# Optimization experiments

Hardware: AMD Instinct MI355X
Metric: run time of the kernel (lower is better)

The kernel has to match this reference:

```python
import jax, jax.numpy as jnp
import numpy as np

# ----- static configuration (from init_kwargs) -----
M = 129                      # NpointsMesh (odd)
XLIMS = (0.0, 2.0 * np.pi)
L = abs(XLIMS[1] - XLIMS[0])
TAU = 12.0 * (L / (2.0 * np.pi * M)) ** 2
MU0 = 1.0
MU1 = 1.0
PI = np.pi

_kGrid = (2.0 * np.pi / L) * np.linspace(-(M // 2), M // 2, M).astype(np.float32)
_KY, _KX = np.meshgrid(_kGrid, _kGrid)            # tf.meshgrid 'xy': ky[i,j]=k[j], kx[i,j]=k[i]
KX = jnp.asarray(_KX, jnp.float32)
KY = jnp.asarray(_KY, jnp.float32)
_xGrid = np.linspace(XLIMS[0], XLIMS[1], M + 1)[:-1].astype(np.float32)
_YG, _XG = np.meshgrid(_xGrid, _xGrid)
XG = jnp.asarray(_XG, jnp.float32)
YG = jnp.asarray(_YG, jnp.float32)


def gaussian_per(x, tau=TAU, Lp=L):
    # periodic Gaussian: main image + two periodic images
    inv = 1.0 / (4.0 * tau)
    return (jnp.exp(-jnp.square(x) * inv)
            + jnp.exp(-jnp.square(x - Lp) * inv)
            + jnp.exp(-jnp.square(x + Lp) * inv))


def setup_inputs() -> dict:
    key = jax.random.key(0)
    kx, = jax.random.split(key, 1)
    B, NP = 4, 512
    x = jax.random.uniform(kx, (B, NP, 2), dtype=jnp.float32) * L  # points in [0, 2pi)
    ones = jnp.ones((1,), jnp.float32)
    return {"x": x, "shift0": ones, "shift1": ones, "amp0": ones, "amp1": ones}


def reference(x, shift0, shift1, amp0, amp1):
    # Gaussian spreading onto the mesh: [B, Np, M, M]
    diffx = x[:, :, 0][..., None, None] - XG
    diffy = x[:, :, 1][..., None, None] - YG
    g = gaussian_per(diffx) * gaussian_per(diffy)

    # NUFFT: FFT of spread Gaussians, centered spectrum
    G = jnp.fft.fftshift(jnp.fft.fft2(g.astype(jnp.complex64)), axes=(-2, -1))
    # deconvolution of the Gaussian window
    deconv = (PI / TAU) * jnp.exp((jnp.square(KX) + jnp.square(KY)) * TAU)  # [M,M] real
    rfft = G * deconv

    k2 = jnp.square(KX) + jnp.square(KY)
    scale = 1.0 / ((2.0 * PI * M / L) ** 2) / ((2.0 * PI) ** 2) / 2.0

    def channel_energy(amp, shift, mu):
        mult = amp * 4.0 * PI / (k2 + jnp.square(mu * shift))   # [M,M] real (broadcast of [1])
        mfft = rfft * mult * deconv                              # second deconvolution
        irfft = jnp.real(jnp.fft.ifft2(jnp.fft.ifftshift(mfft, axes=(-2, -1)))) * scale
        diag = jnp.sum(irfft * g, axis=(-2, -1))                             # [B, Np]
        total = jnp.sum(jnp.sum(irfft, axis=1, keepdims=True) * g, axis=(-2, -1))
        return total - diag

    e1 = channel_energy(amp0, shift0, MU0)
    e2 = channel_energy(amp1, shift1, MU1)
    return jnp.stack([e1, e2], axis=-1)   # [B, Np, 2]
```

## Files before the change

### kernel.cpp

```cpp
#include <hip/hip_runtime.h>
#include <math.h>

#define MM 129
#define KP 132
#define NP 512
#define NB 4
#define NPC 16
#define PCHUNK (NP / NPC)

static constexpr double D_PI  = 3.14159265358979323846;
static constexpr double D_L   = 2.0 * D_PI;
static constexpr double D_TAU = 12.0 / ((double)MM * (double)MM);
static constexpr double D_INV4TAU = 1.0 / (4.0 * D_TAU);
static constexpr double D_F = 1.0 / (8.0 * D_PI * D_PI * (double)MM * (double)MM * (double)MM * (double)MM);

__device__ __forceinline__ void cmac(float2& acc, float2 a, float2 b) {
    acc.x = fmaf(a.x, b.x, fmaf(-a.y, b.y, acc.x));
    acc.y = fmaf(a.x, b.y, fmaf( a.y, b.x, acc.y));
}

#define PPB 2
__global__ __launch_bounds__(128) void k_dft(const float* __restrict__ x,
                                             float2* __restrict__ A,
                                             float2* __restrict__ B) {
    const int p0  = blockIdx.x * PPB;
    const int tid = threadIdx.x;

    __shared__ float4 sG[MM];
    __shared__ float red[2][8];

    const float inv4tau = (float)D_INV4TAU;
    const float Lf      = (float)D_L;
    for (int idx = tid; idx < MM * PPB; idx += 128) {
        int pt = idx & 1, a = idx >> 1;
        float x0 = x[(p0 + pt) * 2 + 0];
        float x1 = x[(p0 + pt) * 2 + 1];
        float u  = (float)a * (float)(D_L / MM);
        float d0 = x0 - u, d1 = x1 - u;
        float ga = __expf(-d0 * d0 * inv4tau)
                 + __expf(-(d0 - Lf) * (d0 - Lf) * inv4tau)
                 + __expf(-(d0 + Lf) * (d0 + Lf) * inv4tau);
        float gb = __expf(-d1 * d1 * inv4tau)
                 + __expf(-(d1 - Lf) * (d1 - Lf) * inv4tau)
                 + __expf(-(d1 + Lf) * (d1 + Lf) * inv4tau);
        ((float2*)&sG[a])[pt] = make_float2(ga, gb);
    }
    __syncthreads();

    const int pt = tid & 1;
    const int j  = tid >> 1;
    const int kk = 64 + j;
    const float nf = (float)(-2.0 * D_PI / MM);

    float sw, cw;
    __sincosf(nf * (float)j, &sw, &cw);
    const int step16 = (j * 16) % MM;
    int idx = 0;

    float Ar = 0.f, Ai = 0.f, Br = 0.f, Bi = 0.f;
    for (int c = 0; c < 128; c += 16) {
        float st, ct;
        __sincosf(nf * (float)idx, &st, &ct);
        float tx = ct, ty = st;
        #pragma unroll
        for (int q = 0; q < 16; ++q) {
            float2 g = ((const float2*)&sG[c + q])[pt];
            Ar = fmaf(g.x, tx, Ar); Ai = fmaf(g.x, ty, Ai);
            Br = fmaf(g.y, tx, Br); Bi = fmaf(g.y, ty, Bi);
            float nx = fmaf(tx, cw, -(ty * sw));
            float ny = fmaf(tx, sw,   ty * cw);
            tx = nx; ty = ny;
        }
        idx += step16; if (idx >= MM) idx -= MM;
    }
    {
        float st, ct;
        __sincosf(nf * (float)idx, &st, &ct);
        float2 g = ((const float2*)&sG[128])[pt];
        Ar = fmaf(g.x, ct, Ar); Ai = fmaf(g.x, st, Ai);
        Br = fmaf(g.y, ct, Br); Bi = fmaf(g.y, st, Bi);
    }

    {
        const size_t base = (size_t)(p0 + pt) * KP;
        A[base + kk] = make_float2(Ar, Ai);
        B[base + kk] = make_float2(Br, Bi);
        if (j > 0) {
            A[base + 64 - j] = make_float2(Ar, -Ai);
            B[base + 64 - j] = make_float2(Br, -Bi);
        }
    }

    const int lane = tid & 63, wv = tid >> 6;
    float2 t1, t128;
    {
        int ph = (64 * tid) % MM;
        __sincosf(nf * (float)ph, &t1.y, &t1.x);
        __sincosf(nf * 65.f, &t128.y, &t128.x);
    }
    float4 gt   = sG[tid];
    float4 g128 = sG[128];
    #pragma unroll
    for (int p = 0; p < PPB; ++p) {
        float ga = p ? gt.z : gt.x;
        float gb = p ? gt.w : gt.y;
        float ar = ga * t1.x, ai = ga * t1.y;
        float br = gb * t1.x, bi = gb * t1.y;
        if (tid == 0) {
            float ga8 = p ? g128.z : g128.x;
            float gb8 = p ? g128.w : g128.y;
            ar = fmaf(ga8, t128.x, ar); ai = fmaf(ga8, t128.y, ai);
            br = fmaf(gb8, t128.x, br); bi = fmaf(gb8, t128.y, bi);
        }
        #pragma unroll
        for (int o = 32; o > 0; o >>= 1) {
            ar += __shfl_down(ar, o, 64); ai += __shfl_down(ai, o, 64);
            br += __shfl_down(br, o, 64); bi += __shfl_down(bi, o, 64);
        }
        if (lane == 0) {
            red[wv][p * 4 + 0] = ar; red[wv][p * 4 + 1] = ai;
            red[wv][p * 4 + 2] = br; red[wv][p * 4 + 3] = bi;
        }
    }
    __syncthreads();
    if (tid < 4) {
        int p = tid >> 1, isB = tid & 1;
        float re = red[0][p * 4 + isB * 2 + 0] + red[1][p * 4 + isB * 2 + 0];
        float im = red[0][p * 4 + isB * 2 + 1] + red[1][p * 4 + isB * 2 + 1];
        float2* dst = isB ? B : A;
        const size_t base = (size_t)(p0 + p) * KP;
        dst[base + 128] = make_float2(re, im);
        dst[base + 0]   = make_float2(re, -im);
    }
}

__global__ __launch_bounds__(128) void k_s1(const float2* __restrict__ A,
                                            const float2* __restrict__ B,
                                            float2* __restrict__ P) {
    const int b   = blockIdx.z;
    const int pc  = blockIdx.y;
    const int p0  = pc * PCHUNK;
    const int m0  = blockIdx.x * 4;
    const int tid = threadIdx.x;

    const float2* __restrict__ Ab = A + (size_t)b * NP * KP;
    const float2* __restrict__ Bb = B + (size_t)b * NP * KP;

    float2 acc[4];
    #pragma unroll
    for (int i = 0; i < 4; ++i) acc[i] = make_float2(0.f, 0.f);
    float2 acc2 = make_float2(0.f, 0.f);

    float2 v[4], am[4][4], as[4], bu[4];
    #pragma unroll
    for (int i = 0; i < 4; ++i) {
        const size_t r = (size_t)(p0 + i) * KP;
        v[i]  = Bb[r + tid];
        bu[i] = Bb[r + 128];
        as[i] = Ab[r + m0 + (tid & 3)];
        #pragma unroll
        for (int j = 0; j < 4; ++j) am[i][j] = Ab[r + m0 + j];
    }

    for (int pg = 0; pg < PCHUNK; pg += 4) {
        float2 nv[4], nam[4][4], nas[4], nbu[4];
        const bool more = (pg + 4 < PCHUNK);
        if (more) {
            #pragma unroll
            for (int i = 0; i < 4; ++i) {
                const size_t r = (size_t)(p0 + pg + 4 + i) * KP;
                nv[i]  = Bb[r + tid];
                nbu[i] = Bb[r + 128];
                nas[i] = Ab[r + m0 + (tid & 3)];
                #pragma unroll
                for (int j = 0; j < 4; ++j) nam[i][j] = Ab[r + m0 + j];
            }
        }
        #pragma unroll
        for (int i = 0; i < 4; ++i) {
            cmac(acc[0], am[i][0], v[i]);
            cmac(acc[1], am[i][1], v[i]);
            cmac(acc[2], am[i][2], v[i]);
            cmac(acc[3], am[i][3], v[i]);
        }
        if (tid < 4) {
            #pragma unroll
            for (int i = 0; i < 4; ++i) cmac(acc2, as[i], bu[i]);
        }
        if (more) {
            #pragma unroll
            for (int i = 0; i < 4; ++i) {
                v[i] = nv[i]; bu[i] = nbu[i]; as[i] = nas[i];
                #pragma unroll
                for (int j = 0; j < 4; ++j) am[i][j] = nam[i][j];
            }
        }
    }

    float2* Pb = P + ((size_t)(b * NPC + pc) * 68) * KP;
    #pragma unroll
    for (int i = 0; i < 4; ++i)
        Pb[(size_t)(m0 + i) * KP + tid] = acc[i];
    if (tid < 4)
        Pb[(size_t)(m0 + tid) * KP + 128] = acc2;
}

#define OUT_FLOATS (NB * NP * 2)
__global__ __launch_bounds__(256) void k_s2(const float2* __restrict__ P,
                                            float2* __restrict__ S,
                                            const float* __restrict__ s0p,
                                            const float* __restrict__ s1p,
                                            const float* __restrict__ a0p,
                                            const float* __restrict__ a1p,
                                            float2* __restrict__ Wp,
                                            float* __restrict__ out) {
    const int idx = blockIdx.x * 256 + threadIdx.x;

    if (idx < OUT_FLOATS) out[idx] = 0.f;

    if (idx < 65 * KP) {
        int m = idx / KP, n = idx - (idx / KP) * KP;
        float w0 = 0.f, w1 = 0.f;
        if (n < MM) {
            float kx = (float)(m - 64), ky = (float)(n - 64);
            float k2   = kx * kx + ky * ky;
            float dec  = (float)(D_PI / D_TAU) * expf(k2 * (float)D_TAU);
            float base = dec * dec * (float)(4.0 * D_PI * D_F);
            float s0 = s0p[0], s1 = s1p[0];
            w0 = a0p[0] * base / (k2 + s0 * s0);
            w1 = a1p[0] * base / (k2 + s1 * s1);
        }
        Wp[idx] = make_float2(w0, w1);
    }

    if (idx < NB * 68 * KP) {
        const int b   = idx / (68 * KP);
        const int rem = idx - b * (68 * KP);
        const int m   = rem / KP;
        const int n   = rem - m * KP;
        if (n <= 128) {
            const float2* __restrict__ Pb =
                P + ((size_t)b * NPC * 68) * KP + (size_t)m * KP + n;
            float re = 0.f, im = 0.f;
            #pragma unroll
            for (int pc = 0; pc < NPC; ++pc) {
                float2 vv = Pb[(size_t)pc * 68 * KP];
                re += vv.x; im += vv.y;
            }
            S[(size_t)b * KP * KP + (size_t)m * KP + n] = make_float2(re, im);
        }
    }
}

__global__ __launch_bounds__(128) void k_final(const float2* __restrict__ A,
                                               const float2* __restrict__ B,
                                               const float2* __restrict__ S,
                                               const float2* __restrict__ Wp,
                                               float* __restrict__ out) {
    const int b      = blockIdx.z;
    const int mc     = blockIdx.y;
    const int mstart = mc * 8;
    const int p0     = blockIdx.x * 8;
    const int tid    = threadIdx.x;

    __shared__ float2 sA[8][65];
    __shared__ float2 sB[8][KP];
    for (int idx = tid; idx < 8 * 65; idx += 128) {
        int pi = idx / 65, k = idx - pi * 65;
        sA[pi][k] = A[(size_t)(b * NP + p0 + pi) * KP + k];
    }
    for (int idx = tid; idx < 8 * 129; idx += 128) {
        int pi = idx / 129, k = idx - pi * 129;
        sB[pi][k] = B[(size_t)(b * NP + p0 + pi) * KP + k];
    }
    __syncthreads();

    float2 bb[8];
    #pragma unroll
    for (int pi = 0; pi < 8; ++pi) bb[pi] = sB[pi][tid];

    float e0[8], e1[8];
    #pragma unroll
    for (int i = 0; i < 8; ++i) { e0[i] = 0.f; e1[i] = 0.f; }

    const float2* __restrict__ Sb = S + (size_t)b * KP * KP;
    float2 s = Sb[(size_t)mstart * KP + tid];
    float2 w = Wp[(size_t)mstart * KP + tid];
    #pragma unroll
    for (int mi = 0; mi < 8; ++mi) {
        const int m = mstart + mi;
        float2 sn = s, wn = w;
        if (mi < 7) {
            sn = Sb[(size_t)(m + 1) * KP + tid];
            wn = Wp[(size_t)(m + 1) * KP + tid];
        }
        #pragma unroll
        for (int pi = 0; pi < 8; ++pi) {
            float2 a  = sA[pi][m];
            float2 bv = bb[pi];
            float abr = a.x * bv.x - a.y * bv.y;
            float abi = a.x * bv.y + a.y * bv.x;
            float d   = fmaf(s.x, abr, s.y * abi) - fmaf(abr, abr, abi * abi);
            e0[pi] = fmaf(w.x, d, e0[pi]);
            e1[pi] = fmaf(w.y, d, e1[pi]);
        }
        s = sn; w = wn;
    }
    if (tid < 8) {
        const int m = mstart + tid;
        float2 s8 = Sb[(size_t)m * KP + 128];
        float2 w8 = Wp[(size_t)m * KP + 128];
        #pragma unroll
        for (int pi = 0; pi < 8; ++pi) {
            float2 a  = sA[pi][m];
            float2 bv = sB[pi][128];
            float abr = a.x * bv.x - a.y * bv.y;
            float abi = a.x * bv.y + a.y * bv.x;
            float d   = fmaf(s8.x, abr, s8.y * abi) - fmaf(abr, abr, abi * abi);
            e0[pi] = fmaf(w8.x, d, e0[pi]);
            e1[pi] = fmaf(w8.y, d, e1[pi]);
        }
    }
    #pragma unroll
    for (int i = 0; i < 8; ++i) { e0[i] *= 2.f; e1[i] *= 2.f; }

    if (mc == 7) {
        float wt = (tid < 64) ? 2.f : ((tid == 64) ? 1.f : 0.f);
        float2 s64 = Sb[(size_t)64 * KP + tid];
        float2 w64 = Wp[(size_t)64 * KP + tid];
        w64.x *= wt; w64.y *= wt;
        #pragma unroll
        for (int pi = 0; pi < 8; ++pi) {
            float2 a  = sA[pi][64];
            float2 bv = bb[pi];
            float abr = a.x * bv.x - a.y * bv.y;
            float abi = a.x * bv.y + a.y * bv.x;
            float d   = fmaf(s64.x, abr, s64.y * abi) - fmaf(abr, abr, abi * abi);
            e0[pi] = fmaf(w64.x, d, e0[pi]);
            e1[pi] = fmaf(w64.y, d, e1[pi]);
        }
    }

    const int lane = tid & 63, wv = tid >> 6;
    __shared__ float part[2][16];
    #pragma unroll
    for (int pi = 0; pi < 8; ++pi) {
        float r0 = e0[pi], r1 = e1[pi];
        #pragma unroll
        for (int o = 32; o > 0; o >>= 1) {
            r0 += __shfl_down(r0, o, 64);
            r1 += __shfl_down(r1, o, 64);
        }
        if (lane == 0) { part[wv][pi * 2 + 0] = r0; part[wv][pi * 2 + 1] = r1; }
    }
    __syncthreads();
    if (tid < 16) {
        float r = part[0][tid] + part[1][tid];
        int pi = tid >> 1, c = tid & 1;
        atomicAdd(&out[((size_t)(b * NP + p0 + pi)) * 2 + c], r);
    }
}

extern "C" void kernel_launch(void* const* d_in, const int* in_sizes, int n_in,
                              void* d_out, int out_size, void* d_ws, size_t ws_size,
                              hipStream_t stream) {
    const float* x      = (const float*)d_in[0];
    const float* shift0 = (const float*)d_in[1];
    const float* shift1 = (const float*)d_in[2];
    const float* amp0   = (const float*)d_in[3];
    const float* amp1   = (const float*)d_in[4];
    float* out = (float*)d_out;

    float2* A  = (float2*)d_ws;
    float2* Bv = A + (size_t)NB * NP * KP;
    float2* S  = Bv + (size_t)NB * NP * KP;
    float2* Wp = S + (size_t)NB * KP * KP;
    float2* P  = Wp + (size_t)65 * KP;

    k_dft<<<(NB * NP) / PPB, 128, 0, stream>>>(x, A, Bv);
    k_s1<<<dim3(17, NPC, NB), 128, 0, stream>>>(A, Bv, P);
    k_s2<<<(NB * 68 * KP + 255) / 256, 256, 0, stream>>>(P, S, shift0, shift1,
                                                         amp0, amp1, Wp, out);
    k_final<<<dim3(NP / 8, 8, NB), 128, 0, stream>>>(A, Bv, S, Wp, out);
}
```

Before: 100.2 us.

## Fold reduction kernel into s1 via last-block counter and widen final tiles

Removes the separate k_s2 launch. Output zeroing and weight table setup move into spare threads of k_dft, and the partial-sum reduction into S is done by the last-arriving k_s1 block per column, found with an atomic counter and thread fences. k_final now handles 16 points per block instead of 8 and uses a shared-memory transpose reduction in place of per-point wave shuffles. This saves a launch and a pass over P, at the cost of atomics, fences and more registers in k_final.

```diff
diff --git a/kernel.cpp b/kernel.cpp
--- a/kernel.cpp
+++ b/kernel.cpp
@@ -7,6 +7,8 @@
 #define NB 4
 #define NPC 16
 #define PCHUNK (NP / NPC)
+#define FPB 16
+#define OUT_FLOATS (NB * NP * 2)
 
 static constexpr double D_PI  = 3.14159265358979323846;
 static constexpr double D_L   = 2.0 * D_PI;
@@ -22,9 +24,41 @@
 #define PPB 2
 __global__ __launch_bounds__(128) void k_dft(const float* __restrict__ x,
                                              float2* __restrict__ A,
-                                             float2* __restrict__ B) {
+                                             float2* __restrict__ B,
+                                             const float* __restrict__ s0p,
+                                             const float* __restrict__ s1p,
+                                             const float* __restrict__ a0p,
+                                             const float* __restrict__ a1p,
+                                             float2* __restrict__ Wp,
+                                             float* __restrict__ out,
+                                             int* __restrict__ cnt) {
     const int p0  = blockIdx.x * PPB;
     const int tid = threadIdx.x;
+
+    {
+        const int bx = blockIdx.x;
+        if (bx < 32) {
+            out[bx * 128 + tid] = 0.f;
+        } else if (bx < 100) {
+            int idx = (bx - 32) * 128 + tid;
+            if (idx < 65 * KP) {
+                int m = idx / KP, n = idx - (idx / KP) * KP;
+                float w0 = 0.f, w1 = 0.f;
+                if (n < MM) {
+                    float kx = (float)(m - 64), ky = (float)(n - 64);
+                    float k2   = kx * kx + ky * ky;
+                    float dec  = (float)(D_PI / D_TAU) * expf(k2 * (float)D_TAU);
+                    float base = dec * dec * (float)(4.0 * D_PI * D_F);
+                    float s0 = s0p[0], s1 = s1p[0];
+                    w0 = a0p[0] * base / (k2 + s0 * s0);
+                    w1 = a1p[0] * base / (k2 + s1 * s1);
+                }
+                Wp[idx] = make_float2(w0, w1);
+            }
+        } else if (bx == 100 && tid < 17 * NB) {
+            cnt[tid] = 0;
+        }
+    }
 
     __shared__ float4 sG[MM];
     __shared__ float red[2][8];
@@ -136,7 +170,9 @@
 
 __global__ __launch_bounds__(128) void k_s1(const float2* __restrict__ A,
                                             const float2* __restrict__ B,
-                                            float2* __restrict__ P) {
+                                            float2* __restrict__ P,
+                                            float2* __restrict__ S,
+                                            int* __restrict__ cnt) {
     const int b   = blockIdx.z;
     const int pc  = blockIdx.y;
     const int p0  = pc * PCHUNK;
@@ -203,52 +239,40 @@
         Pb[(size_t)(m0 + i) * KP + tid] = acc[i];
     if (tid < 4)
         Pb[(size_t)(m0 + tid) * KP + 128] = acc2;
-}
-
-#define OUT_FLOATS (NB * NP * 2)
-__global__ __launch_bounds__(256) void k_s2(const float2* __restrict__ P,
-                                            float2* __restrict__ S,
-                                            const float* __restrict__ s0p,
-                                            const float* __restrict__ s1p,
-                                            const float* __restrict__ a0p,
-                                            const float* __restrict__ a1p,
-                                            float2* __restrict__ Wp,
-                                            float* __restrict__ out) {
-    const int idx = blockIdx.x * 256 + threadIdx.x;
-
-    if (idx < OUT_FLOATS) out[idx] = 0.f;
-
-    if (idx < 65 * KP) {
-        int m = idx / KP, n = idx - (idx / KP) * KP;
-        float w0 = 0.f, w1 = 0.f;
-        if (n < MM) {
-            float kx = (float)(m - 64), ky = (float)(n - 64);
-            float k2   = kx * kx + ky * ky;
-            float dec  = (float)(D_PI / D_TAU) * expf(k2 * (float)D_TAU);
-            float base = dec * dec * (float)(4.0 * D_PI * D_F);
-            float s0 = s0p[0], s1 = s1p[0];
-            w0 = a0p[0] * base / (k2 + s0 * s0);
-            w1 = a1p[0] * base / (k2 + s1 * s1);
-        }
-        Wp[idx] = make_float2(w0, w1);
-    }
-
-    if (idx < NB * 68 * KP) {
-        const int b   = idx / (68 * KP);
-        const int rem = idx - b * (68 * KP);
-        const int m   = rem / KP;
-        const int n   = rem - m * KP;
-        if (n <= 128) {
-            const float2* __restrict__ Pb =
-                P + ((size_t)b * NPC * 68) * KP + (size_t)m * KP + n;
-            float re = 0.f, im = 0.f;
-            #pragma unroll
-            for (int pc = 0; pc < NPC; ++pc) {
-                float2 vv = Pb[(size_t)pc * 68 * KP];
-                re += vv.x; im += vv.y;
-            }
-            S[(size_t)b * KP * KP + (size_t)m * KP + n] = make_float2(re, im);
-        }
+
+    __threadfence();
+    __syncthreads();
+    __shared__ int sLast;
+    if (tid == 0) {
+        int vv = atomicAdd(&cnt[b * 17 + blockIdx.x], 1);
+        sLast = ((vv & (NPC - 1)) == NPC - 1) ? 1 : 0;
+    }
+    __syncthreads();
+    if (!sLast) return;
+    __threadfence();
+
+    const float2* __restrict__ Pb0 = P + (size_t)b * NPC * 68 * KP;
+    float2* __restrict__ Sb = S + (size_t)b * KP * KP;
+    #pragma unroll
+    for (int i = 0; i < 4; ++i) {
+        const int m = m0 + i;
+        float re = 0.f, im = 0.f;
+        #pragma unroll
+        for (int q = 0; q < NPC; ++q) {
+            float2 vv = Pb0[((size_t)q * 68 + m) * KP + tid];
+            re += vv.x; im += vv.y;
+        }
+        Sb[(size_t)m * KP + tid] = make_float2(re, im);
+    }
+    if (tid < 4) {
+        const int m = m0 + tid;
+        float re = 0.f, im = 0.f;
+        #pragma unroll
+        for (int q = 0; q < NPC; ++q) {
+            float2 vv = Pb0[((size_t)q * 68 + m) * KP + 128];
+            re += vv.x; im += vv.y;
+        }
+        Sb[(size_t)m * KP + 128] = make_float2(re, im);
     }
 }
 
@@ -260,28 +284,29 @@
     const int b      = blockIdx.z;
     const int mc     = blockIdx.y;
     const int mstart = mc * 8;
-    const int p0     = blockIdx.x * 8;
+    const int p0     = blockIdx.x * FPB;
     const int tid    = threadIdx.x;
 
-    __shared__ float2 sA[8][65];
-    __shared__ float2 sB[8][KP];
-    for (int idx = tid; idx < 8 * 65; idx += 128) {
+    __shared__ float2 sA[FPB][65];
+    __shared__ float2 sB[FPB][KP];
+    __shared__ float segs[4][32];
+    for (int idx = tid; idx < FPB * 65; idx += 128) {
         int pi = idx / 65, k = idx - pi * 65;
         sA[pi][k] = A[(size_t)(b * NP + p0 + pi) * KP + k];
     }
-    for (int idx = tid; idx < 8 * 129; idx += 128) {
+    for (int idx = tid; idx < FPB * 129; idx += 128) {
         int pi = idx / 129, k = idx - pi * 129;
         sB[pi][k] = B[(size_t)(b * NP + p0 + pi) * KP + k];
     }
     __syncthreads();
 
-    float2 bb[8];
-    #pragma unroll
-    for (int pi = 0; pi < 8; ++pi) bb[pi] = sB[pi][tid];
-
-    float e0[8], e1[8];
-    #pragma unroll
-    for (int i = 0; i < 8; ++i) { e0[i] = 0.f; e1[i] = 0.f; }
+    float2 bb[FPB];
+    #pragma unroll
+    for (int pi = 0; pi < FPB; ++pi) bb[pi] = sB[pi][tid];
+
+    float e0[FPB], e1[FPB];
+    #pragma unroll
+    for (int i = 0; i < FPB; ++i) { e0[i] = 0.f; e1[i] = 0.f; }
 
     const float2* __restrict__ Sb = S + (size_t)b * KP * KP;
     float2 s = Sb[(size_t)mstart * KP + tid];
@@ -295,7 +320,7 @@
             wn = Wp[(size_t)(m + 1) * KP + tid];
         }
         #pragma unroll
-        for (int pi = 0; pi < 8; ++pi) {
+        for (int pi = 0; pi < FPB; ++pi) {
             float2 a  = sA[pi][m];
             float2 bv = bb[pi];
             float abr = a.x * bv.x - a.y * bv.y;
@@ -311,7 +336,7 @@
         float2 s8 = Sb[(size_t)m * KP + 128];
         float2 w8 = Wp[(size_t)m * KP + 128];
         #pragma unroll
-        for (int pi = 0; pi < 8; ++pi) {
+        for (int pi = 0; pi < FPB; ++pi) {
             float2 a  = sA[pi][m];
             float2 bv = sB[pi][128];
             float abr = a.x * bv.x - a.y * bv.y;
@@ -322,7 +347,7 @@
         }
     }
     #pragma unroll
-    for (int i = 0; i < 8; ++i) { e0[i] *= 2.f; e1[i] *= 2.f; }
+    for (int i = 0; i < FPB; ++i) { e0[i] *= 2.f; e1[i] *= 2.f; }
 
     if (mc == 7) {
         float wt = (tid < 64) ? 2.f : ((tid == 64) ? 1.f : 0.f);
@@ -330,7 +355,7 @@
         float2 w64 = Wp[(size_t)64 * KP + tid];
         w64.x *= wt; w64.y *= wt;
         #pragma unroll
-        for (int pi = 0; pi < 8; ++pi) {
+        for (int pi = 0; pi < FPB; ++pi) {
             float2 a  = sA[pi][64];
             float2 bv = bb[pi];
             float abr = a.x * bv.x - a.y * bv.y;
@@ -341,21 +366,25 @@
         }
     }
 
-    const int lane = tid & 63, wv = tid >> 6;
-    __shared__ float part[2][16];
-    #pragma unroll
-    for (int pi = 0; pi < 8; ++pi) {
-        float r0 = e0[pi], r1 = e1[pi];
-        #pragma unroll
-        for (int o = 32; o > 0; o >>= 1) {
-            r0 += __shfl_down(r0, o, 64);
-            r1 += __shfl_down(r1, o, 64);
-        }
-        if (lane == 0) { part[wv][pi * 2 + 0] = r0; part[wv][pi * 2 + 1] = r1; }
-    }
-    __syncthreads();
-    if (tid < 16) {
-        float r = part[0][tid] + part[1][tid];
+    __syncthreads();
+    float* part = (float*)&sB[0][0];
+    #pragma unroll
+    for (int pi = 0; pi < FPB; ++pi) {
+        part[tid * 33 + 2 * pi + 0] = e0[pi];
+        part[tid * 33 + 2 * pi + 1] = e1[pi];
+    }
+    __syncthreads();
+    {
+        const int q = tid & 31, seg = tid >> 5;
+        float acc = 0.f;
+        #pragma unroll
+        for (int i = 0; i < 32; ++i)
+            acc += part[(seg * 32 + i) * 33 + q];
+        segs[seg][q] = acc;
+    }
+    __syncthreads();
+    if (tid < 32) {
+        float r = segs[0][tid] + segs[1][tid] + segs[2][tid] + segs[3][tid];
         int pi = tid >> 1, c = tid & 1;
         atomicAdd(&out[((size_t)(b * NP + p0 + pi)) * 2 + c], r);
     }
@@ -376,10 +405,10 @@
     float2* S  = Bv + (size_t)NB * NP * KP;
     float2* Wp = S + (size_t)NB * KP * KP;
     float2* P  = Wp + (size_t)65 * KP;
-
-    k_dft<<<(NB * NP) / PPB, 128, 0, stream>>>(x, A, Bv);
-    k_s1<<<dim3(17, NPC, NB), 128, 0, stream>>>(A, Bv, P);
-    k_s2<<<(NB * 68 * KP + 255) / 256, 256, 0, stream>>>(P, S, shift0, shift1,
-                                                         amp0, amp1, Wp, out);
-    k_final<<<dim3(NP / 8, 8, NB), 128, 0, stream>>>(A, Bv, S, Wp, out);
+    int*    cnt = (int*)(P + (size_t)NB * NPC * 68 * KP);
+
+    k_dft<<<(NB * NP) / PPB, 128, 0, stream>>>(x, A, Bv, shift0, shift1,
+                                               amp0, amp1, Wp, out, cnt);
+    k_s1<<<dim3(17, NPC, NB), 128, 0, stream>>>(A, Bv, P, S, cnt);
+    k_final<<<dim3(NP / FPB, 8, NB), 128, 0, stream>>>(A, Bv, S, Wp, out);
 }
```

Result: slower. 163.4 us (+63.1%).
